# Performance work log

Measured on AMD Instinct MI355X. Metric: run time of the kernel, lower is better.

## Reference

```python
import jax, jax.numpy as jnp
import numpy as np
from jax import lax

WS = 7  # window_size
PAD = WS // 2


def _gaussian_window(window_size, channel, sigma=1.5):
    x = np.arange(window_size, dtype=np.float64)
    g = np.exp(-((x - window_size // 2) ** 2) / (2.0 * sigma ** 2))
    g = g / g.sum()
    w2 = np.outer(g, g).astype(np.float32)  # (ws, ws)
    w = np.broadcast_to(w2[None, None], (channel, 1, window_size, window_size))
    return jnp.asarray(np.ascontiguousarray(w))


def setup_inputs() -> dict:
    key = jax.random.key(0)
    k1, k2, k3 = jax.random.split(key, 3)
    shape = (16, 1, 1024, 1024)
    img1 = jax.random.uniform(k1, shape, dtype=jnp.float32)
    img2 = jax.random.uniform(k2, shape, dtype=jnp.float32)
    img3 = jax.random.uniform(k3, shape, dtype=jnp.float32)
    window = _gaussian_window(WS, channel=1)  # (1,1,7,7) depthwise Gaussian
    return {"img1": img1, "img2": img2, "img3": img3, "window": window}


def _dwconv(x, window, channel):
    # depthwise conv2d, SAME-style padding = ws//2, groups = channel
    return lax.conv_general_dilated(
        x, window, window_strides=(1, 1), padding=[(PAD, PAD), (PAD, PAD)],
        dimension_numbers=("NCHW", "OIHW", "NCHW"), feature_group_count=channel)


def reference(img1, img2, img3, window):
    channel = img1.shape[1]
    conv = lambda x: _dwconv(x, window, channel)

    mu1 = conv(img1)
    mu2 = conv(img2)
    mu3 = conv(img3)

    sigma1_sq = conv(img1 * img1) - mu1 * mu1
    sigma2_sq = conv(img2 * img2) - mu2 * mu2
    sigma3_sq = conv(img3 * img3) - mu3 * mu3
    sigma12 = conv(img1 * img2) - mu1 * mu2
    sigma13 = conv(img1 * img3) - mu1 * mu3

    C2 = 0.03 ** 2
    ssim_map_12 = (2.0 * sigma12 + C2) / (sigma1_sq + sigma2_sq + C2)
    ssim_map_13 = (2.0 * sigma13 + C2) / (sigma1_sq + sigma3_sq + C2)

    # size_average=True branch
    ssim_map = jnp.where(mu2 > mu3, ssim_map_12, ssim_map_13)
    return jnp.mean(ssim_map)
```

## Files before the change

kernel.cpp:

```cpp
#include <hip/hip_runtime.h>

typedef float v2f __attribute__((ext_vector_type(2)));

#define W 1024
#define H 1024
#define NB 16
#define TX 32
#define TY 26
#define HR 32
#define NTH 256
#define YBLK ((H + TY - 1) / TY)
#define RSTRIDE (4 * TX * 2)

template <int TALL>
__device__ __forceinline__ float vconv_ssim(
    const float* __restrict__ hbuf, int base, const float* __restrict__ g,
    int gy0 )
{
    v2f sv[4][TALL];
    #pragma unroll
    for (int cp = 0; cp < 4; ++cp)
        #pragma unroll
        for (int j = 0; j < TALL; ++j) sv[cp][j] = (v2f)0.0f;

    #pragma unroll
    for (int dy = 0; dy < TALL + 6; ++dy) {
        v2f p[4];
        #pragma unroll
        for (int cp = 0; cp < 4; ++cp)
            p[cp] = *(const v2f*)&hbuf[base + dy * RSTRIDE + cp * 64];
        #pragma unroll
        for (int j = 0; j < TALL; ++j) {
            const int dd = dy - j;
            if (dd >= 0 && dd < 7) {
                const float wg = g[dd];
                #pragma unroll
                for (int cp = 0; cp < 4; ++cp) sv[cp][j] += wg * p[cp];
            }
        }
    }

    float lsum = 0.0f;
    #pragma unroll
    for (int j = 0; j < TALL; ++j) {
        if (gy0 + j < H) {
            const float mu1 = sv[0][j].x, mu2 = sv[0][j].y;
            const float mu3 = sv[1][j].x, E11 = sv[1][j].y;
            const float E22 = sv[2][j].x, E33 = sv[2][j].y;
            const float E12 = sv[3][j].x, E13 = sv[3][j].y;
            const float sig1  = E11 - mu1 * mu1;
            const float sig2  = E22 - mu2 * mu2;
            const float sig3  = E33 - mu3 * mu3;
            const float sig12 = E12 - mu1 * mu2;
            const float sig13 = E13 - mu1 * mu3;
            const float C2 = 9.0e-4f;
            const float m12 = (2.0f * sig12 + C2) * __builtin_amdgcn_rcpf(sig1 + sig2 + C2);
            const float m13 = (2.0f * sig13 + C2) * __builtin_amdgcn_rcpf(sig1 + sig3 + C2);
            lsum += (mu2 > mu3) ? m12 : m13;
        }
    }
    return lsum;
}

__global__ __launch_bounds__(NTH, 4) void ssim_main(
    const float* __restrict__ img1, const float* __restrict__ img2,
    const float* __restrict__ img3, const float* __restrict__ win,
    float* __restrict__ partial)
{
    __shared__ __align__(16) float hbuf[HR * RSTRIDE];

    const int tid = threadIdx.x;
    const int x0  = blockIdx.x * TX;
    const int ys0 = blockIdx.y * TY;
    const size_t imoff = (size_t)blockIdx.z * (size_t)(W * H);
    const float* p1 = img1 + imoff;
    const float* p2 = img2 + imoff;
    const float* p3 = img3 + imoff;

    float g[7];
    {
        const float inv = 1.0f / sqrtf(win[24]);
        #pragma unroll
        for (int j = 0; j < 7; ++j) g[j] = win[21 + j] * inv;
    }

    {
        const int br  = tid >> 3;
        const int bc0 = (tid & 7) << 2;
        const int gy  = ys0 + br - 3;
        const int gx0 = x0 + bc0 - 4;
        const bool xfast = (gx0 >= 0) & (gx0 + 12 <= W);

        v2f accA[8], accB[8];
        #pragma unroll
        for (int ch = 0; ch < 8; ++ch) { accA[ch] = (v2f)0.0f; accB[ch] = (v2f)0.0f; }

        if ((gy >= 0) & (gy < H)) {
            const size_t rowoff = (size_t)gy * W;
            float V1[12], V2[12], V3[12];
            if (xfast) {
                const float* q1 = p1 + rowoff + gx0;
                const float* q2 = p2 + rowoff + gx0;
                const float* q3 = p3 + rowoff + gx0;
                *(float4*)&V1[0] = *(const float4*)(q1);
                *(float4*)&V1[4] = *(const float4*)(q1 + 4);
                *(float4*)&V1[8] = *(const float4*)(q1 + 8);
                *(float4*)&V2[0] = *(const float4*)(q2);
                *(float4*)&V2[4] = *(const float4*)(q2 + 4);
                *(float4*)&V2[8] = *(const float4*)(q2 + 8);
                *(float4*)&V3[0] = *(const float4*)(q3);
                *(float4*)&V3[4] = *(const float4*)(q3 + 4);
                *(float4*)&V3[8] = *(const float4*)(q3 + 8);
            } else {
                #pragma unroll
                for (int c = 0; c < 12; ++c) {
                    const int x = gx0 + c;
                    const bool ok = (x >= 0) & (x < W);
                    const size_t off = rowoff + x;
                    V1[c] = ok ? p1[off] : 0.0f;
                    V2[c] = ok ? p2[off] : 0.0f;
                    V3[c] = ok ? p3[off] : 0.0f;
                }
            }

            v2f gp[8];
            gp[0] = (v2f){g[0], 0.0f};
            #pragma unroll
            for (int m = 2; m <= 7; ++m) gp[m - 1] = (v2f){g[m - 1], g[m - 2]};
            gp[7] = (v2f){0.0f, g[6]};

            #pragma unroll
            for (int m = 1; m <= 8; ++m) {
                const v2f w = gp[m - 1];
                const float vA1 = V1[m], vA2 = V2[m], vA3 = V3[m];
                const float vB1 = V1[m + 2], vB2 = V2[m + 2], vB3 = V3[m + 2];
                v2f t;
                t = w * vA1;
                accA[0] += t;
                accA[3] += t * vA1;
                accA[6] += t * vA2;
                accA[7] += t * vA3;
                t = w * vA2;
                accA[1] += t;
                accA[4] += t * vA2;
                t = w * vA3;
                accA[2] += t;
                accA[5] += t * vA3;
                t = w * vB1;
                accB[0] += t;
                accB[3] += t * vB1;
                accB[6] += t * vB2;
                accB[7] += t * vB3;
                t = w * vB2;
                accB[1] += t;
                accB[4] += t * vB2;
                t = w * vB3;
                accB[2] += t;
                accB[5] += t * vB3;
            }
        }
        const int wbase = br * RSTRIDE + bc0 * 2;
        #pragma unroll
        for (int cp = 0; cp < 4; ++cp) {
            float* d = &hbuf[wbase + cp * 64];
            v2f q;
            q.x = accA[2 * cp].x; q.y = accA[2 * cp + 1].x; *(v2f*)(d + 0) = q;
            q.x = accA[2 * cp].y; q.y = accA[2 * cp + 1].y; *(v2f*)(d + 2) = q;
            q.x = accB[2 * cp].x; q.y = accB[2 * cp + 1].x; *(v2f*)(d + 4) = q;
            q.x = accB[2 * cp].y; q.y = accB[2 * cp + 1].y; *(v2f*)(d + 6) = q;
        }
    }
    __syncthreads();

    const int tx = tid & 31;
    float lsum;
    if (tid < 192) {
        const int r0 = (tid >> 5) * 3;
        lsum = vconv_ssim<3>(hbuf, r0 * RSTRIDE + tx * 2, g, ys0 + r0);
    } else {
        const int r0 = 18 + (((tid >> 5) - 6) << 2);
        lsum = vconv_ssim<4>(hbuf, r0 * RSTRIDE + tx * 2, g, ys0 + r0);
    }

    #pragma unroll
    for (int o = 32; o > 0; o >>= 1) lsum += __shfl_down(lsum, o, 64);
    __syncthreads();
    float* wavesum = hbuf;
    if ((tid & 63) == 0) wavesum[tid >> 6] = lsum;
    __syncthreads();
    if (tid == 0) {
        const float t = (wavesum[0] + wavesum[1]) + (wavesum[2] + wavesum[3]);
        partial[((size_t)blockIdx.z * gridDim.y + blockIdx.y) * gridDim.x + blockIdx.x] = t;
    }
}

__global__ __launch_bounds__(256) void ssim_reduce(
    const float* __restrict__ partial, float* __restrict__ out, int n)
{
    __shared__ double sh[256];
    const int tid = threadIdx.x;
    double s = 0.0;
    for (int i = tid; i < n; i += 256) s += (double)partial[i];
    sh[tid] = s;
    __syncthreads();
    for (int o = 128; o > 0; o >>= 1) {
        if (tid < o) sh[tid] += sh[tid + o];
        __syncthreads();
    }
    if (tid == 0) out[0] = (float)(sh[0] / (double)((size_t)NB * W * H));
}

extern "C" void kernel_launch(void* const* d_in, const int* in_sizes, int n_in,
                              void* d_out, int out_size, void* d_ws, size_t ws_size,
                              hipStream_t stream) {
    const float* img1 = (const float*)d_in[0];
    const float* img2 = (const float*)d_in[1];
    const float* img3 = (const float*)d_in[2];
    const float* win  = (const float*)d_in[3];
    float* out = (float*)d_out;
    float* partial = (float*)d_ws;

    dim3 grid(W / TX, YBLK, NB);
    ssim_main<<<grid, NTH, 0, stream>>>(img1, img2, img3, win, partial);

    const int nblk = (W / TX) * YBLK * NB;
    ssim_reduce<<<1, 256, 0, stream>>>(partial, out, nblk);
}
```

Baseline: 122.7 us.

## Shrink row tile, switch to channel-planar LDS layout, raise occupancy

Reduces the tile height from 26 to 20 output rows (26 halo rows), so the shared buffer is smaller. Launch bounds go from 4 to 6 blocks per SIMD unit to allow more resident waves. The intermediate LDS layout becomes channel-planar with scalar reads and plain stores, and the vertical pass is rebalanced into groups of 3 and 2 rows. In exchange the halo overhead per output row rises (26/20 vs 32/26), and the tighter register budget may cause spills.

```diff
diff --git a/kernel.cpp b/kernel.cpp
--- a/kernel.cpp
+++ b/kernel.cpp
@@ -6,11 +6,11 @@
 #define H 1024
 #define NB 16
 #define TX 32
-#define TY 26
-#define HR 32
+#define TY 20
+#define HR 26
 #define NTH 256
 #define YBLK ((H + TY - 1) / TY)
-#define RSTRIDE (4 * TX * 2)
+#define RSTRIDE (8 * TX)
 
 template <int TALL>
 __device__ __forceinline__ float vconv_ssim(
@@ -27,8 +27,10 @@
     for (int dy = 0; dy < TALL + 6; ++dy) {
         v2f p[4];
         #pragma unroll
-        for (int cp = 0; cp < 4; ++cp)
-            p[cp] = *(const v2f*)&hbuf[base + dy * RSTRIDE + cp * 64];
+        for (int cp = 0; cp < 4; ++cp) {
+            p[cp].x = hbuf[base + cp * 64];
+            p[cp].y = hbuf[base + cp * 64 + 32];
+        }
         #pragma unroll
         for (int j = 0; j < TALL; ++j) {
             const int dd = dy - j;
@@ -38,6 +40,7 @@
                 for (int cp = 0; cp < 4; ++cp) sv[cp][j] += wg * p[cp];
             }
         }
+        base += RSTRIDE;
     }
 
     float lsum = 0.0f;
@@ -62,7 +65,7 @@
     return lsum;
 }
 
-__global__ __launch_bounds__(NTH, 4) void ssim_main(
+__global__ __launch_bounds__(NTH, 6) void ssim_main(
     const float* __restrict__ img1, const float* __restrict__ img2,
     const float* __restrict__ img3, const float* __restrict__ win,
     float* __restrict__ partial)
@@ -84,7 +87,7 @@
         for (int j = 0; j < 7; ++j) g[j] = win[21 + j] * inv;
     }
 
-    {
+    if (tid < HR * 8) {
         const int br  = tid >> 3;
         const int bc0 = (tid & 7) << 2;
         const int gy  = ys0 + br - 3;
@@ -159,27 +162,24 @@
                 accB[5] += t * vB3;
             }
         }
-        const int wbase = br * RSTRIDE + bc0 * 2;
-        #pragma unroll
-        for (int cp = 0; cp < 4; ++cp) {
-            float* d = &hbuf[wbase + cp * 64];
-            v2f q;
-            q.x = accA[2 * cp].x; q.y = accA[2 * cp + 1].x; *(v2f*)(d + 0) = q;
-            q.x = accA[2 * cp].y; q.y = accA[2 * cp + 1].y; *(v2f*)(d + 2) = q;
-            q.x = accB[2 * cp].x; q.y = accB[2 * cp + 1].x; *(v2f*)(d + 4) = q;
-            q.x = accB[2 * cp].y; q.y = accB[2 * cp + 1].y; *(v2f*)(d + 6) = q;
+        const int wbase = br * RSTRIDE + bc0;
+        #pragma unroll
+        for (int ch = 0; ch < 8; ++ch) {
+            *(v2f*)&hbuf[wbase + ch * TX]     = accA[ch];
+            *(v2f*)&hbuf[wbase + ch * TX + 2] = accB[ch];
         }
     }
     __syncthreads();
 
     const int tx = tid & 31;
+    const int grp = tid >> 5;
     float lsum;
-    if (tid < 192) {
-        const int r0 = (tid >> 5) * 3;
-        lsum = vconv_ssim<3>(hbuf, r0 * RSTRIDE + tx * 2, g, ys0 + r0);
+    if (grp < 4) {
+        const int r0 = grp * 3;
+        lsum = vconv_ssim<3>(hbuf, r0 * RSTRIDE + tx, g, ys0 + r0);
     } else {
-        const int r0 = 18 + (((tid >> 5) - 6) << 2);
-        lsum = vconv_ssim<4>(hbuf, r0 * RSTRIDE + tx * 2, g, ys0 + r0);
+        const int r0 = 12 + ((grp - 4) << 1);
+        lsum = vconv_ssim<2>(hbuf, r0 * RSTRIDE + tx, g, ys0 + r0);
     }
 
     #pragma unroll
```

After: 187.3 us. 52.6% more time.
